# Performance work log

Hardware: AMD Instinct MI355X
Metric: run time of the kernel (lower is better)

Reference implementation:

```python
import jax, jax.numpy as jnp
import numpy as np

HEADS = 12
EMBED = 768
HEAD_DIM = EMBED // HEADS


def setup_inputs() -> dict:
    key = jax.random.key(0)
    kx, kw, kb = jax.random.split(key, 3)
    x = jax.random.normal(kx, (8, 1024, EMBED), dtype=jnp.float32)
    # nn.Linear(embed, 3*embed): weight (3E, E), bias (3E,)
    W_qkv = jax.random.normal(kw, (3 * EMBED, EMBED), dtype=jnp.float32) * (1.0 / np.sqrt(EMBED))
    b_qkv = jax.random.normal(kb, (3 * EMBED,), dtype=jnp.float32) * 0.01
    return {"x": x, "W_qkv": W_qkv, "b_qkv": b_qkv}


def reference(x, W_qkv, b_qkv):
    b, n, e = x.shape
    qkv = x @ W_qkv.T + b_qkv                       # (b, n, 3E)
    qkv = qkv.reshape(b, n, HEADS, 3 * HEAD_DIM)    # (b, n, h, 3d)
    q, k, v = jnp.split(qkv, 3, axis=-1)            # each (b, n, h, d)
    scores = jnp.einsum('bihd,bjhd->bijh', q, k) / np.sqrt(HEAD_DIM)
    attn = jax.nn.softmax(scores, axis=-2)          # softmax over keys j (dim=-2)
    out = jnp.einsum('bijh,bjhd->bihd', attn, v)
    return out.reshape(b, n, e)
```

## Files before the change

kernel.cpp:

```cpp
#include <hip/hip_runtime.h>
#include <hip/hip_bf16.h>
#include <cstdint>
#include <math.h>

#define BATCH 8
#define SEQ   1024
#define EMB   768
#define HEADS 12
#define HDIM  64
#define C3    2304
#define MROWS (BATCH*SEQ)
#define NKT   (EMB / 32)
#define MTILES (MROWS / 128)
#define NTILES (C3 / 128)
#define XPACK_BLOCKS (MTILES * NKT)
#define WPACK_BLOCKS (NTILES * NKT)

typedef __attribute__((ext_vector_type(8)))  short bf16x8;
typedef __attribute__((ext_vector_type(4)))  short bf16x4;
typedef __attribute__((ext_vector_type(4)))  float f32x4;
typedef __attribute__((ext_vector_type(16))) float f32x16;

static __device__ inline short f2bf(float f) {
    union { float f; uint32_t u; } v; v.f = f;
    uint32_t u = v.u + 0x7fff + ((v.u >> 16) & 1);
    return (short)(u >> 16);
}

static __device__ inline short bfc(float f) {
    __hip_bfloat16 h = __float2bfloat16(f);
    union { __hip_bfloat16 h; short s; } u; u.h = h;
    return u.s;
}

static __device__ __forceinline__ void gload_lds16(const short* g, short* l) {
    __builtin_amdgcn_global_load_lds(
        (const __attribute__((address_space(1))) unsigned int*)g,
        (__attribute__((address_space(3))) unsigned int*)l, 16, 0, 0);
}

__global__ __launch_bounds__(256) void pack_bf16(const float* __restrict__ x,
                                                 short* __restrict__ xb2,
                                                 const float* __restrict__ W,
                                                 short* __restrict__ Wb2) {
    const float* in;
    short* out;
    int blk;
    if (blockIdx.x < XPACK_BLOCKS) {
        in = x; out = xb2; blk = blockIdx.x;
    } else {
        in = W; out = Wb2; blk = blockIdx.x - XPACK_BLOCKS;
    }
    const int mt = blk / NKT;
    const int kt = blk % NKT;
    short* obase = out + (size_t)blk * 4096;

    #pragma unroll
    for (int p = 0; p < 2; ++p) {
        int idx = p * 256 + threadIdx.x;
        int r = idx >> 2, s = idx & 3;
        const float* src = in + (size_t)(mt * 128 + r) * EMB + kt * 32 + s * 8;
        float4 v0 = ((const float4*)src)[0];
        float4 v1 = ((const float4*)src)[1];
        bf16x8 o = { f2bf(v0.x), f2bf(v0.y), f2bf(v0.z), f2bf(v0.w),
                     f2bf(v1.x), f2bf(v1.y), f2bf(v1.z), f2bf(v1.w) };
        int S = ((4 * r + s) ^ (r & 7));
        *(bf16x8*)(obase + S * 8) = o;
    }
}

__global__ __launch_bounds__(256) void qkv_gemm_mfma(const short* __restrict__ Apk,
                                                     const short* __restrict__ Bpk,
                                                     const float* __restrict__ bias,
                                                     short* __restrict__ qkvb) {
    __shared__ short As[2][4096];
    __shared__ short Bs[2][4096];

    const int g    = blockIdx.x;
    const int xcd  = g & 7;
    const int ring = g >> 3;
    const int by   = xcd * 8 + (ring & 7);
    const int bx   = ring >> 3;

    const int t    = threadIdx.x;
    const int w    = t >> 6;
    const int lane = t & 63;
    const int s4   = lane >> 4;
    const int r15  = lane & 15;
    const int m0 = by * 128, n0 = bx * 128;
    const int wm = (w & 1) * 64, wn = (w >> 1) * 64;

    const short* Ab = Apk + (size_t)by * (NKT * 4096);
    const short* Bb = Bpk + (size_t)bx * (NKT * 4096);

    int offA[4], offB[4];
    #pragma unroll
    for (int i = 0; i < 4; ++i) {
        int ra = wm + i * 16 + r15;
        offA[i] = ((4 * ra + s4) ^ (ra & 7)) << 3;
        int rb = wn + i * 16 + r15;
        offB[i] = ((4 * rb + s4) ^ (rb & 7)) << 3;
    }

    const int seg0 = w * 2;

#define STAGE(buf, kt) do {                                                   \
        const short* _a = Ab + (size_t)(kt) * 4096;                           \
        const short* _b = Bb + (size_t)(kt) * 4096;                           \
        gload_lds16(_a + (seg0    ) * 512 + lane * 8, &As[buf][(seg0    ) * 512]); \
        gload_lds16(_b + (seg0    ) * 512 + lane * 8, &Bs[buf][(seg0    ) * 512]); \
        gload_lds16(_a + (seg0 + 1) * 512 + lane * 8, &As[buf][(seg0 + 1) * 512]); \
        gload_lds16(_b + (seg0 + 1) * 512 + lane * 8, &Bs[buf][(seg0 + 1) * 512]); \
    } while (0)

    f32x4 acc[4][4] = {};

#define COMPUTE(buf) do {                                                     \
        bf16x8 af[4], bff[4];                                                 \
        _Pragma("unroll")                                                     \
        for (int i = 0; i < 4; ++i) {                                         \
            af[i]  = *(const bf16x8*)&As[buf][offA[i]];                       \
            bff[i] = *(const bf16x8*)&Bs[buf][offB[i]];                       \
        }                                                                     \
        _Pragma("unroll")                                                     \
        for (int mi = 0; mi < 4; ++mi)                                        \
            _Pragma("unroll")                                                 \
            for (int ni = 0; ni < 4; ++ni)                                    \
                acc[mi][ni] = __builtin_amdgcn_mfma_f32_16x16x32_bf16(        \
                    af[mi], bff[ni], acc[mi][ni], 0, 0, 0);                   \
    } while (0)

    STAGE(0, 0);
    __syncthreads();

    for (int kt = 0; kt < NKT; kt += 2) {
        STAGE(1, kt + 1);
        COMPUTE(0);
        __syncthreads();
        if (kt + 2 < NKT) STAGE(0, kt + 2);
        COMPUTE(1);
        __syncthreads();
    }
#undef STAGE
#undef COMPUTE

    const float QSCL = 0.18033688011112042f;
    float bsv[4], scl[4];
    #pragma unroll
    for (int ni = 0; ni < 4; ++ni) {
        int n = n0 + wn + ni * 16 + r15;
        bsv[ni] = bias[n];
        scl[ni] = ((n % 192) < 64) ? QSCL : 1.0f;
    }
    #pragma unroll
    for (int mi = 0; mi < 4; ++mi)
        #pragma unroll
        for (int ni = 0; ni < 4; ++ni) {
            int n = n0 + wn + ni * 16 + r15;
            #pragma unroll
            for (int reg = 0; reg < 4; ++reg) {
                int m = m0 + wm + mi * 16 + s4 * 4 + reg;
                qkvb[(size_t)m * C3 + n] = f2bf((acc[mi][ni][reg] + bsv[ni]) * scl[ni]);
            }
        }
}

__global__ __launch_bounds__(256) void v_transpose(const short* __restrict__ qkvb,
                                                   short* __restrict__ vt) {
    __shared__ int Lt[64][65];

    const int bh = blockIdx.x;
    const int jt = blockIdx.y;
    const int b = bh / HEADS, h = bh % HEADS;
    const int t = threadIdx.x;
    const int j0 = jt * 64;
    const size_t base = (size_t)b * SEQ * C3 + (size_t)h * 192 + 128;

    #pragma unroll
    for (int p = 0; p < 2; ++p) {
        int idx = p * 256 + t;
        int j = idx >> 3, d0 = (idx & 7) * 8;
        bf16x8 v = *(const bf16x8*)(qkvb + base + (size_t)(j0 + j) * C3 + d0);
        #pragma unroll
        for (int u = 0; u < 8; ++u)
            Lt[d0 + u][j] = (int)(unsigned short)v[u];
    }
    __syncthreads();
    #pragma unroll
    for (int p = 0; p < 2; ++p) {
        int idx = p * 256 + t;
        int d = idx >> 3, c8 = (idx & 7) * 8;
        bf16x8 o;
        #pragma unroll
        for (int u = 0; u < 8; ++u)
            o[u] = (short)Lt[d][c8 + u];
        *(bf16x8*)(vt + ((size_t)bh * 64 + d) * SEQ + j0 + c8) = o;
    }
}

__global__ __launch_bounds__(256, 3) void attn_mfma(const short* __restrict__ qkvb,
                                                    const short* __restrict__ vt,
                                                    float* __restrict__ out) {
    __shared__ short Ks[64][64];
    __shared__ short Vt[64][64];
    __shared__ short Ps[128][64];

    const int g    = blockIdx.x;
    const int qt   = g / (BATCH * HEADS);
    const int bh   = g % (BATCH * HEADS);
    const int b    = bh / HEADS;
    const int h    = bh % HEADS;
    const int t    = threadIdx.x;
    const int w    = t >> 6;
    const int lane = t & 63;
    const int c    = lane & 15;
    const int q    = lane >> 4;
    const int ck   = c & 7;
    const int i0   = qt * 128;

    const size_t base = (size_t)b * SEQ * C3 + (size_t)h * 192;
    const short* vtb = vt + (size_t)bh * 64 * SEQ;
    const short* gk  = qkvb + base + 64;

    bf16x8 aq[2][2];
    {
        const short* pq = qkvb + base + (size_t)(i0 + w * 32 + c) * C3 + q * 8;
        aq[0][0] = *(const bf16x8*)(pq);
        aq[0][1] = *(const bf16x8*)(pq + 32);
        aq[1][0] = *(const bf16x8*)(pq + (size_t)16 * C3);
        aq[1][1] = *(const bf16x8*)(pq + (size_t)16 * C3 + 32);
    }

    const int jA = t >> 3;
    const int jB = jA + 32;
    const int sg = t & 7;
    const int wKA = (sg ^ (jA & 7)) * 8;
    const int wKB = (sg ^ (jB & 7)) * 8;

    bf16x8 kr0, kr1, vr0, vr1;
    kr0 = *(const bf16x8*)(gk + (size_t)jA * C3 + sg * 8);
    kr1 = *(const bf16x8*)(gk + (size_t)jB * C3 + sg * 8);
    vr0 = *(const bf16x8*)(vtb + (size_t)jA * SEQ + sg * 8);
    vr1 = *(const bf16x8*)(vtb + (size_t)jB * SEQ + sg * 8);

    f32x4 o[2][4] = {};
    float l_acc[2] = {0.f, 0.f};

    for (int kt = 0; kt < 16; ++kt) {
        __syncthreads();
        *(bf16x8*)&Ks[jA][wKA] = kr0;
        *(bf16x8*)&Ks[jB][wKB] = kr1;
        *(bf16x8*)&Vt[jA][wKA] = vr0;
        *(bf16x8*)&Vt[jB][wKB] = vr1;
        __syncthreads();

        if (kt < 15) {
            const int j0 = (kt + 1) * 64;
            kr0 = *(const bf16x8*)(gk + (size_t)(j0 + jA) * C3 + sg * 8);
            kr1 = *(const bf16x8*)(gk + (size_t)(j0 + jB) * C3 + sg * 8);
            vr0 = *(const bf16x8*)(vtb + (size_t)jA * SEQ + j0 + sg * 8);
            vr1 = *(const bf16x8*)(vtb + (size_t)jB * SEQ + j0 + sg * 8);
        }

        bf16x8 ka[4][2];
        #pragma unroll
        for (int mt = 0; mt < 4; ++mt) {
            ka[mt][0] = *(bf16x8*)&Ks[mt * 16 + c][(q ^ ck) * 8];
            ka[mt][1] = *(bf16x8*)&Ks[mt * 16 + c][((4 + q) ^ ck) * 8];
        }

        f32x4 s[2][4];
        #pragma unroll
        for (int ss = 0; ss < 2; ++ss)
            #pragma unroll
            for (int mt = 0; mt < 4; ++mt) {
                f32x4 acc = {0.f, 0.f, 0.f, 0.f};
                acc = __builtin_amdgcn_mfma_f32_16x16x32_bf16(ka[mt][0], aq[ss][0], acc, 0, 0, 0);
                acc = __builtin_amdgcn_mfma_f32_16x16x32_bf16(ka[mt][1], aq[ss][1], acc, 0, 0, 0);
                s[ss][mt] = acc;
            }

        #pragma unroll
        for (int ss = 0; ss < 2; ++ss)
            #pragma unroll
            for (int mt = 0; mt < 4; ++mt) {
                float p0 = exp2f(s[ss][mt][0]);
                float p1 = exp2f(s[ss][mt][1]);
                float p2 = exp2f(s[ss][mt][2]);
                float p3 = exp2f(s[ss][mt][3]);
                l_acc[ss] += (p0 + p1) + (p2 + p3);
                bf16x4 pw = { bfc(p0), bfc(p1), bfc(p2), bfc(p3) };
                int pcol = (((2 * mt + (q >> 1)) ^ ck) << 3) + (q & 1) * 4;
                *(bf16x4*)&Ps[w * 32 + ss * 16 + c][pcol] = pw;
            }

        bf16x8 vb[4][2];
        #pragma unroll
        for (int dt = 0; dt < 4; ++dt) {
            vb[dt][0] = *(bf16x8*)&Vt[dt * 16 + c][(q ^ ck) * 8];
            vb[dt][1] = *(bf16x8*)&Vt[dt * 16 + c][((4 + q) ^ ck) * 8];
        }

        #pragma unroll
        for (int ss = 0; ss < 2; ++ss) {
            bf16x8 ap0 = *(bf16x8*)&Ps[w * 32 + ss * 16 + c][(q ^ ck) * 8];
            bf16x8 ap1 = *(bf16x8*)&Ps[w * 32 + ss * 16 + c][((4 + q) ^ ck) * 8];
            #pragma unroll
            for (int dt = 0; dt < 4; ++dt) {
                o[ss][dt] = __builtin_amdgcn_mfma_f32_16x16x32_bf16(ap0, vb[dt][0], o[ss][dt], 0, 0, 0);
                o[ss][dt] = __builtin_amdgcn_mfma_f32_16x16x32_bf16(ap1, vb[dt][1], o[ss][dt], 0, 0, 0);
            }
        }
    }

    float linv[2][4];
    #pragma unroll
    for (int ss = 0; ss < 2; ++ss) {
        float v = l_acc[ss];
        v += __shfl_xor(v, 16, 64);
        v += __shfl_xor(v, 32, 64);
        #pragma unroll
        for (int r = 0; r < 4; ++r)
            linv[ss][r] = 1.0f / __shfl(v, 4 * q + r, 64);
    }

    #pragma unroll
    for (int ss = 0; ss < 2; ++ss)
        #pragma unroll
        for (int dt = 0; dt < 4; ++dt)
            #pragma unroll
            for (int r = 0; r < 4; ++r) {
                int i = w * 32 + ss * 16 + q * 4 + r;
                out[((size_t)b * SEQ + i0 + i) * EMB + h * HDIM + dt * 16 + c]
                    = o[ss][dt][r] * linv[ss][r];
            }
}

extern "C" void kernel_launch(void* const* d_in, const int* in_sizes, int n_in,
                              void* d_out, int out_size, void* d_ws, size_t ws_size,
                              hipStream_t stream) {
    const float* x    = (const float*)d_in[0];
    const float* W    = (const float*)d_in[1];
    const float* bias = (const float*)d_in[2];
    float* out = (float*)d_out;

    short* xb2  = (short*)d_ws;
    short* Wb2  = xb2 + (size_t)MROWS * EMB;
    short* qkvb = Wb2 + (size_t)C3 * EMB;
    short* vt   = qkvb + (size_t)MROWS * C3;

    pack_bf16<<<XPACK_BLOCKS + WPACK_BLOCKS, 256, 0, stream>>>(x, xb2, W, Wb2);

    qkv_gemm_mfma<<<1152, 256, 0, stream>>>(xb2, Wb2, bias, qkvb);

    dim3 g2(BATCH * HEADS, SEQ / 64);
    v_transpose<<<g2, 256, 0, stream>>>(qkvb, vt);

    attn_mfma<<<BATCH * HEADS * (SEQ / 128), 256, 0, stream>>>(qkvb, vt, out);
}
```

Before: 169.2 us.

## Halve attention query tile to 64 rows, raise occupancy, use natural exp

Shrinks each attention block's query tile from 128 to 64 rows, so each wave handles 16 query rows instead of 32. The grid doubles, the P buffer in LDS halves, and launch bounds rise to 6 blocks per CU to improve latency hiding. Q scaling changes from log2e/sqrt(d) with exp2f to 1/sqrt(d) with __expf, and P conversion uses the manual rounding helper. MFMA sections are wrapped in s_setprio. The cost is that K/V tiles are loaded and staged twice as often per query, raising global and LDS traffic.

```diff
diff --git a/kernel.cpp b/kernel.cpp
--- a/kernel.cpp
+++ b/kernel.cpp
@@ -19,18 +19,11 @@
 typedef __attribute__((ext_vector_type(8)))  short bf16x8;
 typedef __attribute__((ext_vector_type(4)))  short bf16x4;
 typedef __attribute__((ext_vector_type(4)))  float f32x4;
-typedef __attribute__((ext_vector_type(16))) float f32x16;
 
 static __device__ inline short f2bf(float f) {
     union { float f; uint32_t u; } v; v.f = f;
     uint32_t u = v.u + 0x7fff + ((v.u >> 16) & 1);
     return (short)(u >> 16);
-}
-
-static __device__ inline short bfc(float f) {
-    __hip_bfloat16 h = __float2bfloat16(f);
-    union { __hip_bfloat16 h; short s; } u; u.h = h;
-    return u.s;
 }
 
 static __device__ __forceinline__ void gload_lds16(const short* g, short* l) {
@@ -144,13 +137,12 @@
 #undef STAGE
 #undef COMPUTE
 
-    const float QSCL = 0.18033688011112042f;
     float bsv[4], scl[4];
     #pragma unroll
     for (int ni = 0; ni < 4; ++ni) {
         int n = n0 + wn + ni * 16 + r15;
         bsv[ni] = bias[n];
-        scl[ni] = ((n % 192) < 64) ? QSCL : 1.0f;
+        scl[ni] = ((n % 192) < 64) ? 0.125f : 1.0f;
     }
     #pragma unroll
     for (int mi = 0; mi < 4; ++mi)
@@ -198,12 +190,12 @@
     }
 }
 
-__global__ __launch_bounds__(256, 3) void attn_mfma(const short* __restrict__ qkvb,
+__global__ __launch_bounds__(256, 6) void attn_mfma(const short* __restrict__ qkvb,
                                                     const short* __restrict__ vt,
                                                     float* __restrict__ out) {
     __shared__ short Ks[64][64];
     __shared__ short Vt[64][64];
-    __shared__ short Ps[128][64];
+    __shared__ short Ps[64][64];
 
     const int g    = blockIdx.x;
     const int qt   = g / (BATCH * HEADS);
@@ -216,19 +208,17 @@
     const int c    = lane & 15;
     const int q    = lane >> 4;
     const int ck   = c & 7;
-    const int i0   = qt * 128;
+    const int i0   = qt * 64;
 
     const size_t base = (size_t)b * SEQ * C3 + (size_t)h * 192;
     const short* vtb = vt + (size_t)bh * 64 * SEQ;
     const short* gk  = qkvb + base + 64;
 
-    bf16x8 aq[2][2];
+    bf16x8 aq0, aq1;
     {
-        const short* pq = qkvb + base + (size_t)(i0 + w * 32 + c) * C3 + q * 8;
-        aq[0][0] = *(const bf16x8*)(pq);
-        aq[0][1] = *(const bf16x8*)(pq + 32);
-        aq[1][0] = *(const bf16x8*)(pq + (size_t)16 * C3);
-        aq[1][1] = *(const bf16x8*)(pq + (size_t)16 * C3 + 32);
+        const short* pq = qkvb + base + (size_t)(i0 + w * 16 + c) * C3 + q * 8;
+        aq0 = *(const bf16x8*)(pq);
+        aq1 = *(const bf16x8*)(pq + 32);
     }
 
     const int jA = t >> 3;
@@ -243,8 +233,8 @@
     vr0 = *(const bf16x8*)(vtb + (size_t)jA * SEQ + sg * 8);
     vr1 = *(const bf16x8*)(vtb + (size_t)jB * SEQ + sg * 8);
 
-    f32x4 o[2][4] = {};
-    float l_acc[2] = {0.f, 0.f};
+    f32x4 o[4] = {};
+    float l_acc = 0.f;
 
     for (int kt = 0; kt < 16; ++kt) {
         __syncthreads();
@@ -269,30 +259,28 @@
             ka[mt][1] = *(bf16x8*)&Ks[mt * 16 + c][((4 + q) ^ ck) * 8];
         }
 
-        f32x4 s[2][4];
-        #pragma unroll
-        for (int ss = 0; ss < 2; ++ss)
-            #pragma unroll
-            for (int mt = 0; mt < 4; ++mt) {
-                f32x4 acc = {0.f, 0.f, 0.f, 0.f};
-                acc = __builtin_amdgcn_mfma_f32_16x16x32_bf16(ka[mt][0], aq[ss][0], acc, 0, 0, 0);
-                acc = __builtin_amdgcn_mfma_f32_16x16x32_bf16(ka[mt][1], aq[ss][1], acc, 0, 0, 0);
-                s[ss][mt] = acc;
-            }
-
-        #pragma unroll
-        for (int ss = 0; ss < 2; ++ss)
-            #pragma unroll
-            for (int mt = 0; mt < 4; ++mt) {
-                float p0 = exp2f(s[ss][mt][0]);
-                float p1 = exp2f(s[ss][mt][1]);
-                float p2 = exp2f(s[ss][mt][2]);
-                float p3 = exp2f(s[ss][mt][3]);
-                l_acc[ss] += (p0 + p1) + (p2 + p3);
-                bf16x4 pw = { bfc(p0), bfc(p1), bfc(p2), bfc(p3) };
-                int pcol = (((2 * mt + (q >> 1)) ^ ck) << 3) + (q & 1) * 4;
-                *(bf16x4*)&Ps[w * 32 + ss * 16 + c][pcol] = pw;
-            }
+        f32x4 s[4];
+        __builtin_amdgcn_s_setprio(1);
+        #pragma unroll
+        for (int mt = 0; mt < 4; ++mt) {
+            f32x4 acc = {0.f, 0.f, 0.f, 0.f};
+            acc = __builtin_amdgcn_mfma_f32_16x16x32_bf16(ka[mt][0], aq0, acc, 0, 0, 0);
+            acc = __builtin_amdgcn_mfma_f32_16x16x32_bf16(ka[mt][1], aq1, acc, 0, 0, 0);
+            s[mt] = acc;
+        }
+        __builtin_amdgcn_s_setprio(0);
+
+        #pragma unroll
+        for (int mt = 0; mt < 4; ++mt) {
+            float p0 = __expf(s[mt][0]);
+            float p1 = __expf(s[mt][1]);
+            float p2 = __expf(s[mt][2]);
+            float p3 = __expf(s[mt][3]);
+            l_acc += (p0 + p1) + (p2 + p3);
+            bf16x4 pw = { f2bf(p0), f2bf(p1), f2bf(p2), f2bf(p3) };
+            int pcol = (((2 * mt + (q >> 1)) ^ ck) << 3) + (q & 1) * 4;
+            *(bf16x4*)&Ps[w * 16 + c][pcol] = pw;
+        }
 
         bf16x8 vb[4][2];
         #pragma unroll
@@ -301,39 +289,33 @@
             vb[dt][1] = *(bf16x8*)&Vt[dt * 16 + c][((4 + q) ^ ck) * 8];
         }
 
-        #pragma unroll
-        for (int ss = 0; ss < 2; ++ss) {
-            bf16x8 ap0 = *(bf16x8*)&Ps[w * 32 + ss * 16 + c][(q ^ ck) * 8];
-            bf16x8 ap1 = *(bf16x8*)&Ps[w * 32 + ss * 16 + c][((4 + q) ^ ck) * 8];
-            #pragma unroll
-            for (int dt = 0; dt < 4; ++dt) {
-                o[ss][dt] = __builtin_amdgcn_mfma_f32_16x16x32_bf16(ap0, vb[dt][0], o[ss][dt], 0, 0, 0);
-                o[ss][dt] = __builtin_amdgcn_mfma_f32_16x16x32_bf16(ap1, vb[dt][1], o[ss][dt], 0, 0, 0);
-            }
-        }
-    }
-
-    float linv[2][4];
-    #pragma unroll
-    for (int ss = 0; ss < 2; ++ss) {
-        float v = l_acc[ss];
-        v += __shfl_xor(v, 16, 64);
-        v += __shfl_xor(v, 32, 64);
-        #pragma unroll
-        for (int r = 0; r < 4; ++r)
-            linv[ss][r] = 1.0f / __shfl(v, 4 * q + r, 64);
-    }
-
-    #pragma unroll
-    for (int ss = 0; ss < 2; ++ss)
-        #pragma unroll
-        for (int dt = 0; dt < 4; ++dt)
-            #pragma unroll
-            for (int r = 0; r < 4; ++r) {
-                int i = w * 32 + ss * 16 + q * 4 + r;
-                out[((size_t)b * SEQ + i0 + i) * EMB + h * HDIM + dt * 16 + c]
-                    = o[ss][dt][r] * linv[ss][r];
-            }
+        bf16x8 ap0 = *(bf16x8*)&Ps[w * 16 + c][(q ^ ck) * 8];
+        bf16x8 ap1 = *(bf16x8*)&Ps[w * 16 + c][((4 + q) ^ ck) * 8];
+        __builtin_amdgcn_s_setprio(1);
+        #pragma unroll
+        for (int dt = 0; dt < 4; ++dt) {
+            o[dt] = __builtin_amdgcn_mfma_f32_16x16x32_bf16(ap0, vb[dt][0], o[dt], 0, 0, 0);
+            o[dt] = __builtin_amdgcn_mfma_f32_16x16x32_bf16(ap1, vb[dt][1], o[dt], 0, 0, 0);
+        }
+        __builtin_amdgcn_s_setprio(0);
+    }
+
+    float v = l_acc;
+    v += __shfl_xor(v, 16, 64);
+    v += __shfl_xor(v, 32, 64);
+    float linv[4];
+    #pragma unroll
+    for (int r = 0; r < 4; ++r)
+        linv[r] = 1.0f / __shfl(v, 4 * q + r, 64);
+
+    #pragma unroll
+    for (int dt = 0; dt < 4; ++dt)
+        #pragma unroll
+        for (int r = 0; r < 4; ++r) {
+            int i = w * 16 + q * 4 + r;
+            out[((size_t)b * SEQ + i0 + i) * EMB + h * HDIM + dt * 16 + c]
+                = o[dt][r] * linv[r];
+        }
 }
 
 extern "C" void kernel_launch(void* const* d_in, const int* in_sizes, int n_in,
@@ -356,5 +338,5 @@
     dim3 g2(BATCH * HEADS, SEQ / 64);
     v_transpose<<<g2, 256, 0, stream>>>(qkvb, vt);
 
-    attn_mfma<<<BATCH * HEADS * (SEQ / 128), 256, 0, stream>>>(qkvb, vt, out);
-}
+    attn_mfma<<<BATCH * HEADS * (SEQ / 64), 256, 0, stream>>>(qkvb, vt, out);
+}
```

New measurement: 283.0 us. 1.67x slower.
